# Kernel optimization log

Hardware: AMD Instinct MI355X
Metric: run time of the kernel (lower is better)

Reference implementation:

```python
import jax, jax.numpy as jnp
import numpy as np

DIM = 1024
NUM_HEADS = 16
HEAD_DIM = 64  # DIM // NUM_HEADS
BATCH = 2
SEQ = 2048


def setup_inputs() -> dict:
    key = jax.random.key(0)
    ks = jax.random.split(key, 6)
    x = jax.random.normal(ks[0], (BATCH, SEQ, DIM), dtype=jnp.float32)
    # Linear weights stored as [in, out] so y = x @ W (same math as torch Linear).
    Wq = jax.random.normal(ks[1], (DIM, DIM), dtype=jnp.float32) * (DIM ** -0.5)
    # MQA: single shared KV head of size HEAD_DIM.
    Wk = jax.random.normal(ks[2], (DIM, HEAD_DIM), dtype=jnp.float32) * (DIM ** -0.5)
    Wv = jax.random.normal(ks[3], (DIM, HEAD_DIM), dtype=jnp.float32) * (DIM ** -0.5)
    Wo = jax.random.normal(ks[4], (DIM, DIM), dtype=jnp.float32) * (DIM ** -0.5)
    bo = jax.random.normal(ks[5], (DIM,), dtype=jnp.float32) * 0.01
    return {"x": x, "Wq": Wq, "Wk": Wk, "Wv": Wv, "Wo": Wo, "bo": bo}


def reference(x, Wq, Wk, Wv, Wo, bo):
    b, s, _ = x.shape
    scale = HEAD_DIM ** -0.5
    # Per-head queries [b, h, s, d]
    q = (x @ Wq).reshape(b, s, NUM_HEADS, HEAD_DIM).transpose(0, 2, 1, 3) * scale
    # Shared single KV head [b, s, d]
    k = x @ Wk
    v = x @ Wv
    # Materialized scores [b, h, s_q, s_k]
    scores = jnp.einsum('bhqd,bkd->bhqk', q, k)
    causal = jnp.tril(jnp.ones((s, s), dtype=bool))  # True where allowed
    scores = jnp.where(causal, scores, -jnp.inf)
    # Manual stable softmax (max, exp, sum, div) as in the original
    max_scores = jnp.max(scores, axis=-1, keepdims=True)
    exp_scores = jnp.exp(scores - max_scores)
    attn = exp_scores / jnp.sum(exp_scores, axis=-1, keepdims=True)
    out = jnp.einsum('bhqk,bkd->bhqd', attn, v)  # [b, h, s, d]
    out = out.transpose(0, 2, 1, 3).reshape(b, s, DIM)
    return out @ Wo + bo
```

## Files before the change

kernel.cpp:

```cpp
#include <hip/hip_runtime.h>

typedef unsigned short u16;
typedef __attribute__((ext_vector_type(8))) short short8;
typedef __attribute__((ext_vector_type(4))) float f32x4;

static __device__ __forceinline__ u16 f32_to_bf16(float f) {
  unsigned u = __float_as_uint(f);
  u += 0x7fffu + ((u >> 16) & 1u);
  return (u16)(u >> 16);
}

static __device__ __forceinline__ void async16(u16* lds, const u16* g) {
  __builtin_amdgcn_global_load_lds(
      (const __attribute__((address_space(1))) void*)g,
      (__attribute__((address_space(3))) void*)lds, 16, 0, 0);
}


__global__ void __launch_bounds__(256) convert_kernel(
    const float* __restrict__ x, u16* __restrict__ Xb) {
  int t = blockIdx.x * 256 + threadIdx.x;
  int base = t * 8;
  float4 a = *(const float4*)&x[base];
  float4 b = *(const float4*)&x[base + 4];
  short8 v;
  v[0] = (short)f32_to_bf16(a.x); v[1] = (short)f32_to_bf16(a.y);
  v[2] = (short)f32_to_bf16(a.z); v[3] = (short)f32_to_bf16(a.w);
  v[4] = (short)f32_to_bf16(b.x); v[5] = (short)f32_to_bf16(b.y);
  v[6] = (short)f32_to_bf16(b.z); v[7] = (short)f32_to_bf16(b.w);
  *(short8*)&Xb[base] = v;
}

__global__ void __launch_bounds__(256) transpose_kernel(
    const float* __restrict__ Wq, const float* __restrict__ Wk,
    const float* __restrict__ Wv, const float* __restrict__ Wo,
    u16* __restrict__ WqT, u16* __restrict__ WkvT, u16* __restrict__ WoT) {
  __shared__ u16 T[64][72];
  int id = blockIdx.x;
  const float* src; u16* dst; int tk, tn, src_ld, row_off;
  if (id < 256)      { src = Wq; dst = WqT;  tk = id & 15;  tn = id >> 4; src_ld = 1024; row_off = 0; }
  else if (id < 512) { int i = id - 256; src = Wo; dst = WoT; tk = i & 15; tn = i >> 4; src_ld = 1024; row_off = 0; }
  else if (id < 528) { src = Wk; dst = WkvT; tk = id - 512; tn = 0; src_ld = 64; row_off = 0; }
  else               { src = Wv; dst = WkvT; tk = id - 528; tn = 0; src_ld = 64; row_off = 64; }
  int k0 = tk * 64, n0 = tn * 64;
  int tid = threadIdx.x;
#pragma unroll
  for (int it = 0; it < 2; ++it) {
    int c = tid + it * 256;
    int r = c >> 3, cc = (c & 7) * 8;
    const float* p = &src[(k0 + r) * src_ld + n0 + cc];
    float4 a = *(const float4*)&p[0];
    float4 b = *(const float4*)&p[4];
    short8 v;
    v[0] = (short)f32_to_bf16(a.x); v[1] = (short)f32_to_bf16(a.y);
    v[2] = (short)f32_to_bf16(a.z); v[3] = (short)f32_to_bf16(a.w);
    v[4] = (short)f32_to_bf16(b.x); v[5] = (short)f32_to_bf16(b.y);
    v[6] = (short)f32_to_bf16(b.z); v[7] = (short)f32_to_bf16(b.w);
    *(short8*)&T[r][cc] = v;
  }
  __syncthreads();
#pragma unroll
  for (int it = 0; it < 2; ++it) {
    int c = tid + it * 256;
    int r = c >> 3, cc = (c & 7) * 8;
    short8 v;
#pragma unroll
    for (int j = 0; j < 8; ++j) v[j] = (short)T[cc + j][r];
    *(short8*)&dst[(row_off + n0 + r) * 1024 + k0 + cc] = v;
  }
}

__device__ __forceinline__ void gemm_core_128(
    const u16* __restrict__ A, const u16* __restrict__ BT, int m0, int K,
    f32x4 (&acc)[4][4], u16* As, u16* Bs,
    int lane, int w, int wr, int wc, int g, int lo) {
  int lrow = lane >> 3;
  int swz8 = ((lane & 7) ^ lrow) * 8;
  int lo7 = lo & 7;
  for (int k0 = 0; k0 < K; k0 += 64) {
#pragma unroll
    for (int it = 0; it < 4; ++it) {
      int W = w * 4 + it;
      int row = W * 8 + lrow;
      async16(As + W * 512, &A[(size_t)(m0 + row) * K + k0 + swz8]);
      async16(Bs + W * 512, &BT[(size_t)row * K + k0 + swz8]);
    }
    __syncthreads();
#pragma unroll
    for (int ks = 0; ks < 2; ++ks) {
      short8 af[4], bf[4];
#pragma unroll
      for (int i = 0; i < 4; ++i) {
        int pc = ((ks * 4 + g) ^ lo7) * 8;
        af[i] = *(const short8*)&As[(wr * 64 + i * 16 + lo) * 64 + pc];
        bf[i] = *(const short8*)&Bs[(wc * 64 + i * 16 + lo) * 64 + pc];
      }
#pragma unroll
      for (int mi = 0; mi < 4; ++mi)
#pragma unroll
        for (int ni = 0; ni < 4; ++ni)
          acc[mi][ni] = __builtin_amdgcn_mfma_f32_16x16x32_bf16(
              af[mi], bf[ni], acc[mi][ni], 0, 0, 0);
    }
    __syncthreads();
  }
}

__global__ void __launch_bounds__(256) qkv_gemm(
    const u16* __restrict__ Xb, const u16* __restrict__ WqT,
    const u16* __restrict__ WkvT, u16* __restrict__ Qb, u16* __restrict__ KVb,
    u16* __restrict__ VTb) {
  __shared__ u16 As[128 * 64];
  __shared__ u16 Bs[128 * 64];
  int tid = threadIdx.x, lane = tid & 63, w = tid >> 6;
  int wr = w >> 1, wc = w & 1, g = lane >> 4, lo = lane & 15;
  int m0 = blockIdx.x * 128, nb = blockIdx.y;
  const u16* BT = (nb < 8) ? (WqT + (size_t)nb * 128 * 1024) : WkvT;
  f32x4 acc[4][4];
  f32x4 zz = {0.f, 0.f, 0.f, 0.f};
#pragma unroll
  for (int i = 0; i < 4; ++i)
#pragma unroll
    for (int j = 0; j < 4; ++j) acc[i][j] = zz;
  gemm_core_128(Xb, BT, m0, 1024, acc, As, Bs, lane, w, wr, wc, g, lo);
#pragma unroll
  for (int mi = 0; mi < 4; ++mi)
#pragma unroll
    for (int ni = 0; ni < 4; ++ni)
#pragma unroll
      for (int r = 0; r < 4; ++r) {
        int row = m0 + wr * 64 + mi * 16 + g * 4 + r;
        int col = wc * 64 + ni * 16 + lo;
        u16 v = f32_to_bf16(acc[mi][ni][r]);
        if (nb < 8) {
          Qb[row * 1024 + nb * 128 + col] = v;
        } else if (wc == 0) {
          KVb[row * 64 + col] = v;
        } else {
          int d = col - 64;
          VTb[(((row >> 11) * 64) + d) * 2048 + (row & 2047)] = v;
        }
      }
}

__global__ void __launch_bounds__(256, 4) attn_kernel(
    const u16* __restrict__ Qb, const u16* __restrict__ KVb,
    const u16* __restrict__ VTb, u16* __restrict__ AOb) {
  __shared__ u16 Ks[64 * 64];
  __shared__ u16 Vt[64 * 64];
  __shared__ u16 Ps[4][16][72];
  int tid = threadIdx.x, lane = tid & 63, w = tid >> 6;
  int g = lane >> 4, lo = lane & 15;
  int h = blockIdx.x;
  int by = blockIdx.y;
  int qt = (by < 16) ? by : (47 - by);
  int b = blockIdx.z;
  int q0 = qt * 64;
  int qbase = q0 + w * 16;
  int lrow = lane >> 3;
  int swz8 = ((lane & 7) ^ lrow) * 8;
  int lo7 = lo & 7;

  short8 qf[2];
  {
    const u16* qp = &Qb[(size_t)(b * 2048 + qbase + lo) * 1024 + h * 64];
    qf[0] = *(const short8*)&qp[g * 8];
    qf[1] = *(const short8*)&qp[32 + g * 8];
  }

  short8 ones;
#pragma unroll
  for (int j = 0; j < 8; ++j) ones[j] = (short)0x3F80;

  f32x4 oacc[4], l_acc;
  f32x4 zz = {0.f, 0.f, 0.f, 0.f};
#pragma unroll
  for (int i = 0; i < 4; ++i) oacc[i] = zz;
  l_acc = zz;

  const float kExp = 0.18033688011112042f;
  const float kOff = 11.541560327111707f;

  int ntiles = qt + 1;
  for (int t = 0; t < ntiles; ++t) {
    int k0 = t * 64;
#pragma unroll
    for (int it = 0; it < 2; ++it) {
      int W = w * 2 + it;
      async16(Ks + W * 512, &KVb[(size_t)(b * 2048 + k0 + W * 8 + lrow) * 64 + swz8]);
      async16(Vt + W * 512, &VTb[((size_t)b * 64 + W * 8 + lrow) * 2048 + k0 + swz8]);
    }
    __syncthreads();

    f32x4 sacc[4];
#pragma unroll
    for (int ns = 0; ns < 4; ++ns) sacc[ns] = zz;
#pragma unroll
    for (int ks = 0; ks < 2; ++ks) {
      short8 kf[4];
      int pc = ((ks * 4 + g) ^ lo7) * 8;
#pragma unroll
      for (int ns = 0; ns < 4; ++ns)
        kf[ns] = *(const short8*)&Ks[(ns * 16 + lo) * 64 + pc];
#pragma unroll
      for (int ns = 0; ns < 4; ++ns)
        sacc[ns] = __builtin_amdgcn_mfma_f32_16x16x32_bf16(
            qf[ks], kf[ns], sacc[ns], 0, 0, 0);
    }

    bool need_mask = (k0 + 63) > qbase;
#pragma unroll
    for (int ns = 0; ns < 4; ++ns)
#pragma unroll
      for (int r = 0; r < 4; ++r) {
        float p = __builtin_amdgcn_exp2f(fmaf(sacc[ns][r], kExp, -kOff));
        if (need_mask) {
          int qg = qbase + g * 4 + r;
          int kg = k0 + ns * 16 + lo;
          if (kg > qg) p = 0.f;
        }
        Ps[w][g * 4 + r][ns * 16 + lo] = f32_to_bf16(p);
      }
    __syncthreads();

#pragma unroll
    for (int k2 = 0; k2 < 2; ++k2) {
      short8 pf = *(const short8*)&Ps[w][lo][k2 * 32 + g * 8];
      short8 vf[4];
      int pc = ((k2 * 4 + g) ^ lo7) * 8;
#pragma unroll
      for (int ds = 0; ds < 4; ++ds)
        vf[ds] = *(const short8*)&Vt[(ds * 16 + lo) * 64 + pc];
#pragma unroll
      for (int ds = 0; ds < 4; ++ds)
        oacc[ds] = __builtin_amdgcn_mfma_f32_16x16x32_bf16(
            pf, vf[ds], oacc[ds], 0, 0, 0);
      l_acc = __builtin_amdgcn_mfma_f32_16x16x32_bf16(pf, ones, l_acc, 0, 0, 0);
    }
    __syncthreads();
  }

#pragma unroll
  for (int r = 0; r < 4; ++r) {
    float inv_l = 1.0f / l_acc[r];
    int row = b * 2048 + qbase + g * 4 + r;
#pragma unroll
    for (int ds = 0; ds < 4; ++ds)
      AOb[row * 1024 + h * 64 + ds * 16 + lo] = f32_to_bf16(oacc[ds][r] * inv_l);
  }
}

__global__ void __launch_bounds__(256) out_gemm(
    const u16* __restrict__ A, const u16* __restrict__ WoT,
    const float* __restrict__ bias, float* __restrict__ C) {
  __shared__ u16 As[128 * 64];
  __shared__ u16 Bs[128 * 64];
  int tid = threadIdx.x, lane = tid & 63, w = tid >> 6;
  int wr = w >> 1, wc = w & 1, g = lane >> 4, lo = lane & 15;
  int m0 = blockIdx.x * 128, nb = blockIdx.y;
  const u16* BT = WoT + (size_t)nb * 128 * 1024;
  f32x4 acc[4][4];
  f32x4 zz = {0.f, 0.f, 0.f, 0.f};
#pragma unroll
  for (int i = 0; i < 4; ++i)
#pragma unroll
    for (int j = 0; j < 4; ++j) acc[i][j] = zz;
  gemm_core_128(A, BT, m0, 1024, acc, As, Bs, lane, w, wr, wc, g, lo);
#pragma unroll
  for (int mi = 0; mi < 4; ++mi)
#pragma unroll
    for (int ni = 0; ni < 4; ++ni)
#pragma unroll
      for (int r = 0; r < 4; ++r) {
        int row = m0 + wr * 64 + mi * 16 + g * 4 + r;
        int col = nb * 128 + wc * 64 + ni * 16 + lo;
        C[row * 1024 + col] = acc[mi][ni][r] + bias[col];
      }
}

extern "C" void kernel_launch(void* const* d_in, const int* in_sizes, int n_in,
                              void* d_out, int out_size, void* d_ws, size_t ws_size,
                              hipStream_t stream) {
  const float* x  = (const float*)d_in[0];
  const float* Wq = (const float*)d_in[1];
  const float* Wk = (const float*)d_in[2];
  const float* Wv = (const float*)d_in[3];
  const float* Wo = (const float*)d_in[4];
  const float* bo = (const float*)d_in[5];
  float* out = (float*)d_out;

  u16* ws   = (u16*)d_ws;
  u16* AOb  = ws;
  u16* KVb  = AOb + 4194304;
  u16* VTb  = KVb + 262144;
  u16* Xb   = VTb + 262144;
  u16* WqT  = Xb + 4194304;
  u16* WoT  = WqT + 1048576;
  u16* WkvT = WoT + 1048576;
  u16* Qb   = (u16*)d_out;

  convert_kernel<<<2048, 256, 0, stream>>>(x, Xb);
  transpose_kernel<<<544, 256, 0, stream>>>(Wq, Wk, Wv, Wo, WqT, WkvT, WoT);
  qkv_gemm<<<dim3(32, 9), 256, 0, stream>>>(Xb, WqT, WkvT, Qb, KVb, VTb);
  attn_kernel<<<dim3(16, 32, 2), 256, 0, stream>>>(Qb, KVb, VTb, AOb);
  out_gemm<<<dim3(32, 8), 256, 0, stream>>>(AOb, WoT, bo, out);
}
```

Baseline: 175.9 us.

## Merge prep kernels, shrink GEMM M-tile to 64, relax attention P barrier

Merges the x conversion and weight transpose kernels into one launch. Halves the M tile of the QKV and output GEMMs to 64 rows, doubling the grid to fill more CUs. In attention, the block-wide barrier after writing P is replaced by a block fence, since each wave reads only its own Ps slice. The trade-off is lower per-block reuse of the B tile, and the barrier change depends on intra-wave ordering holding.

After: 160.4 us. 1.1x faster.

```diff
diff --git a/kernel.cpp b/kernel.cpp
--- a/kernel.cpp
+++ b/kernel.cpp
@@ -17,33 +17,34 @@
 }
 
 
-__global__ void __launch_bounds__(256) convert_kernel(
-    const float* __restrict__ x, u16* __restrict__ Xb) {
-  int t = blockIdx.x * 256 + threadIdx.x;
-  int base = t * 8;
-  float4 a = *(const float4*)&x[base];
-  float4 b = *(const float4*)&x[base + 4];
-  short8 v;
-  v[0] = (short)f32_to_bf16(a.x); v[1] = (short)f32_to_bf16(a.y);
-  v[2] = (short)f32_to_bf16(a.z); v[3] = (short)f32_to_bf16(a.w);
-  v[4] = (short)f32_to_bf16(b.x); v[5] = (short)f32_to_bf16(b.y);
-  v[6] = (short)f32_to_bf16(b.z); v[7] = (short)f32_to_bf16(b.w);
-  *(short8*)&Xb[base] = v;
-}
-
-__global__ void __launch_bounds__(256) transpose_kernel(
+__global__ void __launch_bounds__(256) prep_kernel(
+    const float* __restrict__ x,
     const float* __restrict__ Wq, const float* __restrict__ Wk,
     const float* __restrict__ Wv, const float* __restrict__ Wo,
-    u16* __restrict__ WqT, u16* __restrict__ WkvT, u16* __restrict__ WoT) {
+    u16* __restrict__ Xb, u16* __restrict__ WqT, u16* __restrict__ WkvT,
+    u16* __restrict__ WoT) {
   __shared__ u16 T[64][72];
   int id = blockIdx.x;
+  int tid = threadIdx.x;
+  if (id < 2048) {
+    int base = (id * 256 + tid) * 8;
+    float4 a = *(const float4*)&x[base];
+    float4 b = *(const float4*)&x[base + 4];
+    short8 v;
+    v[0] = (short)f32_to_bf16(a.x); v[1] = (short)f32_to_bf16(a.y);
+    v[2] = (short)f32_to_bf16(a.z); v[3] = (short)f32_to_bf16(a.w);
+    v[4] = (short)f32_to_bf16(b.x); v[5] = (short)f32_to_bf16(b.y);
+    v[6] = (short)f32_to_bf16(b.z); v[7] = (short)f32_to_bf16(b.w);
+    *(short8*)&Xb[base] = v;
+    return;
+  }
+  int id2 = id - 2048;
   const float* src; u16* dst; int tk, tn, src_ld, row_off;
-  if (id < 256)      { src = Wq; dst = WqT;  tk = id & 15;  tn = id >> 4; src_ld = 1024; row_off = 0; }
-  else if (id < 512) { int i = id - 256; src = Wo; dst = WoT; tk = i & 15; tn = i >> 4; src_ld = 1024; row_off = 0; }
-  else if (id < 528) { src = Wk; dst = WkvT; tk = id - 512; tn = 0; src_ld = 64; row_off = 0; }
-  else               { src = Wv; dst = WkvT; tk = id - 528; tn = 0; src_ld = 64; row_off = 64; }
+  if (id2 < 256)      { src = Wq; dst = WqT;  tk = id2 & 15; tn = id2 >> 4; src_ld = 1024; row_off = 0; }
+  else if (id2 < 512) { int i = id2 - 256; src = Wo; dst = WoT; tk = i & 15; tn = i >> 4; src_ld = 1024; row_off = 0; }
+  else if (id2 < 528) { src = Wk; dst = WkvT; tk = id2 - 512; tn = 0; src_ld = 64; row_off = 0; }
+  else                { src = Wv; dst = WkvT; tk = id2 - 528; tn = 0; src_ld = 64; row_off = 64; }
   int k0 = tk * 64, n0 = tn * 64;
-  int tid = threadIdx.x;
 #pragma unroll
   for (int it = 0; it < 2; ++it) {
     int c = tid + it * 256;
@@ -70,33 +71,37 @@
   }
 }
 
-__device__ __forceinline__ void gemm_core_128(
+__device__ __forceinline__ void gemm_core_64x128(
     const u16* __restrict__ A, const u16* __restrict__ BT, int m0, int K,
-    f32x4 (&acc)[4][4], u16* As, u16* Bs,
+    f32x4 (&acc)[2][4], u16* As, u16* Bs,
     int lane, int w, int wr, int wc, int g, int lo) {
   int lrow = lane >> 3;
   int swz8 = ((lane & 7) ^ lrow) * 8;
   int lo7 = lo & 7;
   for (int k0 = 0; k0 < K; k0 += 64) {
 #pragma unroll
+    for (int it = 0; it < 2; ++it) {
+      int W = w * 2 + it;
+      async16(As + W * 512, &A[(size_t)(m0 + W * 8 + lrow) * K + k0 + swz8]);
+    }
+#pragma unroll
     for (int it = 0; it < 4; ++it) {
       int W = w * 4 + it;
-      int row = W * 8 + lrow;
-      async16(As + W * 512, &A[(size_t)(m0 + row) * K + k0 + swz8]);
-      async16(Bs + W * 512, &BT[(size_t)row * K + k0 + swz8]);
+      async16(Bs + W * 512, &BT[(size_t)(W * 8 + lrow) * K + k0 + swz8]);
     }
     __syncthreads();
 #pragma unroll
     for (int ks = 0; ks < 2; ++ks) {
-      short8 af[4], bf[4];
-#pragma unroll
-      for (int i = 0; i < 4; ++i) {
-        int pc = ((ks * 4 + g) ^ lo7) * 8;
-        af[i] = *(const short8*)&As[(wr * 64 + i * 16 + lo) * 64 + pc];
+      int pc = ((ks * 4 + g) ^ lo7) * 8;
+      short8 af[2], bf[4];
+#pragma unroll
+      for (int i = 0; i < 2; ++i)
+        af[i] = *(const short8*)&As[(wr * 32 + i * 16 + lo) * 64 + pc];
+#pragma unroll
+      for (int i = 0; i < 4; ++i)
         bf[i] = *(const short8*)&Bs[(wc * 64 + i * 16 + lo) * 64 + pc];
-      }
-#pragma unroll
-      for (int mi = 0; mi < 4; ++mi)
+#pragma unroll
+      for (int mi = 0; mi < 2; ++mi)
 #pragma unroll
         for (int ni = 0; ni < 4; ++ni)
           acc[mi][ni] = __builtin_amdgcn_mfma_f32_16x16x32_bf16(
@@ -110,26 +115,26 @@
     const u16* __restrict__ Xb, const u16* __restrict__ WqT,
     const u16* __restrict__ WkvT, u16* __restrict__ Qb, u16* __restrict__ KVb,
     u16* __restrict__ VTb) {
-  __shared__ u16 As[128 * 64];
+  __shared__ u16 As[64 * 64];
   __shared__ u16 Bs[128 * 64];
   int tid = threadIdx.x, lane = tid & 63, w = tid >> 6;
   int wr = w >> 1, wc = w & 1, g = lane >> 4, lo = lane & 15;
-  int m0 = blockIdx.x * 128, nb = blockIdx.y;
+  int m0 = blockIdx.x * 64, nb = blockIdx.y;
   const u16* BT = (nb < 8) ? (WqT + (size_t)nb * 128 * 1024) : WkvT;
-  f32x4 acc[4][4];
+  f32x4 acc[2][4];
   f32x4 zz = {0.f, 0.f, 0.f, 0.f};
 #pragma unroll
-  for (int i = 0; i < 4; ++i)
+  for (int i = 0; i < 2; ++i)
 #pragma unroll
     for (int j = 0; j < 4; ++j) acc[i][j] = zz;
-  gemm_core_128(Xb, BT, m0, 1024, acc, As, Bs, lane, w, wr, wc, g, lo);
-#pragma unroll
-  for (int mi = 0; mi < 4; ++mi)
+  gemm_core_64x128(Xb, BT, m0, 1024, acc, As, Bs, lane, w, wr, wc, g, lo);
+#pragma unroll
+  for (int mi = 0; mi < 2; ++mi)
 #pragma unroll
     for (int ni = 0; ni < 4; ++ni)
 #pragma unroll
       for (int r = 0; r < 4; ++r) {
-        int row = m0 + wr * 64 + mi * 16 + g * 4 + r;
+        int row = m0 + wr * 32 + mi * 16 + g * 4 + r;
         int col = wc * 64 + ni * 16 + lo;
         u16 v = f32_to_bf16(acc[mi][ni][r]);
         if (nb < 8) {
@@ -221,7 +226,7 @@
         }
         Ps[w][g * 4 + r][ns * 16 + lo] = f32_to_bf16(p);
       }
-    __syncthreads();
+    __threadfence_block();
 
 #pragma unroll
     for (int k2 = 0; k2 < 2; ++k2) {
@@ -253,26 +258,26 @@
 __global__ void __launch_bounds__(256) out_gemm(
     const u16* __restrict__ A, const u16* __restrict__ WoT,
     const float* __restrict__ bias, float* __restrict__ C) {
-  __shared__ u16 As[128 * 64];
+  __shared__ u16 As[64 * 64];
   __shared__ u16 Bs[128 * 64];
   int tid = threadIdx.x, lane = tid & 63, w = tid >> 6;
   int wr = w >> 1, wc = w & 1, g = lane >> 4, lo = lane & 15;
-  int m0 = blockIdx.x * 128, nb = blockIdx.y;
+  int m0 = blockIdx.x * 64, nb = blockIdx.y;
   const u16* BT = WoT + (size_t)nb * 128 * 1024;
-  f32x4 acc[4][4];
+  f32x4 acc[2][4];
   f32x4 zz = {0.f, 0.f, 0.f, 0.f};
 #pragma unroll
-  for (int i = 0; i < 4; ++i)
+  for (int i = 0; i < 2; ++i)
 #pragma unroll
     for (int j = 0; j < 4; ++j) acc[i][j] = zz;
-  gemm_core_128(A, BT, m0, 1024, acc, As, Bs, lane, w, wr, wc, g, lo);
-#pragma unroll
-  for (int mi = 0; mi < 4; ++mi)
+  gemm_core_64x128(A, BT, m0, 1024, acc, As, Bs, lane, w, wr, wc, g, lo);
+#pragma unroll
+  for (int mi = 0; mi < 2; ++mi)
 #pragma unroll
     for (int ni = 0; ni < 4; ++ni)
 #pragma unroll
       for (int r = 0; r < 4; ++r) {
-        int row = m0 + wr * 64 + mi * 16 + g * 4 + r;
+        int row = m0 + wr * 32 + mi * 16 + g * 4 + r;
         int col = nb * 128 + wc * 64 + ni * 16 + lo;
         C[row * 1024 + col] = acc[mi][ni][r] + bias[col];
       }
@@ -299,9 +304,8 @@
   u16* WkvT = WoT + 1048576;
   u16* Qb   = (u16*)d_out;
 
-  convert_kernel<<<2048, 256, 0, stream>>>(x, Xb);
-  transpose_kernel<<<544, 256, 0, stream>>>(Wq, Wk, Wv, Wo, WqT, WkvT, WoT);
-  qkv_gemm<<<dim3(32, 9), 256, 0, stream>>>(Xb, WqT, WkvT, Qb, KVb, VTb);
+  prep_kernel<<<2592, 256, 0, stream>>>(x, Wq, Wk, Wv, Wo, Xb, WqT, WkvT, WoT);
+  qkv_gemm<<<dim3(64, 9), 256, 0, stream>>>(Xb, WqT, WkvT, Qb, KVb, VTb);
   attn_kernel<<<dim3(16, 32, 2), 256, 0, stream>>>(Qb, KVb, VTb, AOb);
-  out_gemm<<<dim3(32, 8), 256, 0, stream>>>(AOb, WoT, bo, out);
-}
+  out_gemm<<<dim3(64, 8), 256, 0, stream>>>(AOb, WoT, bo, out);
+}
```
